# Kernel optimization log

Hardware: AMD Instinct MI355X
Metric: run time of the kernel (lower is better)

## Reference

```python
import jax, jax.numpy as jnp
import numpy as np

HIDDEN = 1024
D_FF = 2816
N_EXPERTS = 8
TOP_K = 2
TEMPERATURE = 1.0
LB_WEIGHT = 0.01


def setup_inputs() -> dict:
    key = jax.random.key(0)
    ks = jax.random.split(key, 5)
    scale_h = 1.0 / np.sqrt(HIDDEN)
    scale_f = 1.0 / np.sqrt(D_FF)
    x = jax.random.normal(ks[0], (2, 1024, HIDDEN), dtype=jnp.float32)
    gate_w = jax.random.normal(ks[1], (N_EXPERTS, HIDDEN), dtype=jnp.float32) * scale_h
    w1 = jax.random.normal(ks[2], (N_EXPERTS, HIDDEN, D_FF), dtype=jnp.float32) * scale_h  # gate proj
    w3 = jax.random.normal(ks[3], (N_EXPERTS, HIDDEN, D_FF), dtype=jnp.float32) * scale_h  # up proj
    w2 = jax.random.normal(ks[4], (N_EXPERTS, D_FF, HIDDEN), dtype=jnp.float32) * scale_f  # down proj
    return {"x": x, "gate_w": gate_w, "w1": w1, "w3": w3, "w2": w2}


def reference(x, gate_w, w1, w3, w2):
    B, S, H = x.shape
    xf = x.reshape(-1, H)                       # [T, H]
    T = xf.shape[0]

    # gating (eval mode: no routing noise)
    gate_logits = xf @ gate_w.T                 # [T, E]
    scaled = gate_logits / TEMPERATURE
    topk_vals, topk_idx = jax.lax.top_k(scaled, TOP_K)   # [T, K]
    topk_probs = jax.nn.softmax(topk_vals, axis=-1)      # [T, K]

    # dense combine weights: weight of expert e for token t (0 if not selected)
    onehot = jax.nn.one_hot(topk_idx, N_EXPERTS, dtype=xf.dtype)  # [T, K, E]
    comb = jnp.einsum("tke,tk->te", onehot, topk_probs)           # [T, E]

    # per-expert SwiGLU on all tokens, masked combine (math equals gather/scatter)
    h1 = jnp.einsum("th,ehf->etf", xf, w1)      # [E, T, F]
    h3 = jnp.einsum("th,ehf->etf", xf, w3)
    act = jax.nn.silu(h1) * h3                  # [E, T, F]
    y = jnp.einsum("etf,efh->eth", act, w2)     # [E, T, H]
    out = jnp.einsum("te,eth->th", comb, y)     # [T, H]

    # auxiliary load-balancing loss
    gate_probs = jax.nn.softmax(gate_logits, axis=-1)             # [T, E]
    expert_usage = onehot.sum(axis=(0, 1)) / (T * TOP_K + 1e-9)   # [E]
    gate_importance = gate_probs.mean(axis=0)                     # [E]
    aux = jnp.sum(expert_usage * gate_importance) * N_EXPERTS
    aux_loss = jnp.minimum(aux * LB_WEIGHT, 1.0)

    return out.reshape(B, S, H), aux_loss
```

## Files before the change

### kernel.cpp

```cpp
#include <hip/hip_runtime.h>
#include <hip/hip_bf16.h>
#include <math.h>


#define T_TOK 2048
#define HID   1024
#define DFF   2816
#define NE    8
#define ROWS  4096

typedef unsigned short u16;
typedef __attribute__((ext_vector_type(8))) short bf16x8;
typedef __attribute__((ext_vector_type(4))) float f32x4;

#define OFF_CNT    0
#define OFF_IMP    64
#define OFF_OFFS   128
#define OFF_TOPKI  256
#define OFF_TOPKP  (OFF_TOPKI + 16384)
#define OFF_BTOK   (OFF_TOPKP + 16384)
#define OFF_EPOS   (OFF_BTOK + 65536)
#define OFF_XB     (OFF_EPOS + 65536)
#define OFF_W1T    (OFF_XB + 4194304)
#define OFF_W3T    (OFF_W1T + 46137344)
#define OFF_W2T    (OFF_W3T + 46137344)
#define OFF_ACT    (OFF_W2T + 46137344)
#define WS_NEEDED  (OFF_ACT + 23068672)

__device__ __forceinline__ u16 f2bf(float f) {
    unsigned u = __float_as_uint(f);
    u = (u + 0x7fffu + ((u >> 16) & 1u)) >> 16;
    return (u16)u;
}

__device__ __forceinline__ void glds16(const void* g, void* l) {
    __builtin_amdgcn_global_load_lds(
        (const __attribute__((address_space(1))) unsigned int*)g,
        (__attribute__((address_space(3))) unsigned int*)l, 16, 0, 0);
}

__global__ void cvt_x_kernel(const float* __restrict__ x, u16* __restrict__ xb) {
    int i = blockIdx.x * 256 + threadIdx.x;
    float4 v = ((const float4*)x)[i];
    union { u16 s[4]; unsigned long long q; } o;
    o.s[0] = f2bf(v.x); o.s[1] = f2bf(v.y); o.s[2] = f2bf(v.z); o.s[3] = f2bf(v.w);
    ((unsigned long long*)xb)[i] = o.q;
}

__global__ void transpose_kernel(const float* __restrict__ in, u16* __restrict__ out,
                                 int K, int N) {
    __shared__ float tile[64][65];
    const float* ip = in + (size_t)blockIdx.z * K * N;
    u16* op = out + (size_t)blockIdx.z * K * N;
    int n0 = blockIdx.x * 64, k0 = blockIdx.y * 64;
    int tid = threadIdx.x;
#pragma unroll
    for (int p = 0; p < 4; ++p) {
        int row = p * 16 + (tid >> 4);
        int v = (tid & 15) * 4;
        float4 d = *(const float4*)(ip + (size_t)(k0 + row) * N + n0 + v);
        tile[row][v] = d.x; tile[row][v + 1] = d.y; tile[row][v + 2] = d.z; tile[row][v + 3] = d.w;
    }
    __syncthreads();
#pragma unroll
    for (int p = 0; p < 2; ++p) {
        int n = p * 32 + (tid >> 3);
        int g = (tid & 7) * 8;
        u16 o[8];
#pragma unroll
        for (int j = 0; j < 8; ++j) o[j] = f2bf(tile[g + j][n]);
        *(bf16x8*)(op + (size_t)(n0 + n) * K + k0 + g) = *(bf16x8*)o;
    }
}

__global__ void gating_kernel(const float* __restrict__ x, const float* __restrict__ gw,
                              int* __restrict__ topki, float* __restrict__ topkp,
                              float* __restrict__ imp) {
    __shared__ float s_imp[NE];
    int tid = threadIdx.x;
    if (tid < NE) s_imp[tid] = 0.f;
    __syncthreads();
    int lane = tid & 63;
    int t = blockIdx.x * 8 + (tid >> 6);
    float a[NE];
#pragma unroll
    for (int e = 0; e < NE; ++e) a[e] = 0.f;
#pragma unroll
    for (int c = 0; c < 16; ++c) {
        float xv = x[(size_t)t * HID + c * 64 + lane];
#pragma unroll
        for (int e = 0; e < NE; ++e) a[e] += xv * gw[e * HID + c * 64 + lane];
    }
#pragma unroll
    for (int e = 0; e < NE; ++e) {
#pragma unroll
        for (int off = 32; off > 0; off >>= 1) a[e] += __shfl_xor(a[e], off, 64);
    }
    if (lane == 0) {
        float v0 = -1e30f, v1 = -1e30f; int e0 = 0, e1 = 0;
#pragma unroll
        for (int e = 0; e < NE; ++e) {
            if (a[e] > v0) { v1 = v0; e1 = e0; v0 = a[e]; e0 = e; }
            else if (a[e] > v1) { v1 = a[e]; e1 = e; }
        }
        float p0 = 1.f / (1.f + expf(v1 - v0));
        topki[2 * t] = e0; topki[2 * t + 1] = e1;
        topkp[2 * t] = p0; topkp[2 * t + 1] = 1.f - p0;
        float s = 0.f, pe[NE];
#pragma unroll
        for (int e = 0; e < NE; ++e) { pe[e] = expf(a[e] - v0); s += pe[e]; }
        float inv = 1.f / s;
#pragma unroll
        for (int e = 0; e < NE; ++e) atomicAdd(&s_imp[e], pe[e] * inv);
    }
    __syncthreads();
    if (tid < NE) atomicAdd(&imp[tid], s_imp[tid]);
}

__global__ void compact_kernel(const int* __restrict__ topki,
                               int* __restrict__ cnt, int* __restrict__ btok,
                               int* __restrict__ epos) {
    int idx = blockIdx.x * 256 + threadIdx.x;
    int e = topki[idx];
    int pos = atomicAdd(&cnt[e], 1);
    btok[e * T_TOK + pos] = idx >> 1;
    epos[idx] = (e << 11) | pos;
}

__global__ void finalize_kernel(const int* __restrict__ cnt, const float* __restrict__ imp,
                                int* __restrict__ offs, float* __restrict__ aux_out) {
    if (threadIdx.x == 0) {
        int off = 0; float s = 0.f;
        for (int e = 0; e < NE; ++e) {
            offs[e] = off; off += cnt[e];
            s += ((float)cnt[e] / (4096.f + 1e-9f)) * (imp[e] / 2048.f);
        }
        aux_out[0] = fminf(s * 8.f * 0.01f, 1.f);
    }
}

__global__ __launch_bounds__(256, 2)
void gemm1_kernel(const u16* __restrict__ xb, const u16* __restrict__ w1t,
                  const u16* __restrict__ w3t, u16* __restrict__ act,
                  const int* __restrict__ btok, const int* __restrict__ cnt,
                  const int* __restrict__ offs) {
    int e = blockIdx.z;
    int n_e = cnt[e];
    int m0 = blockIdx.y * 128;
    if (m0 >= n_e) return;
    int nn0 = blockIdx.x * 128;
    int base = offs[e];

    __shared__ __align__(16) u16 As[128 * 32];
    __shared__ __align__(16) u16 B1s[128 * 32];
    __shared__ __align__(16) u16 B3s[128 * 32];

    int tid = threadIdx.x, lane = tid & 63, wv = tid >> 6;
    int wm = (wv >> 1) * 64, wn = (wv & 1) * 64;
    int l15 = lane & 15, quad = lane >> 4;

    int row0 = tid >> 2, row1 = 64 + row0;
    int q = (tid & 3) ^ ((tid >> 3) & 3);
    int sub = q * 8;
    int t0 = (m0 + row0 < n_e) ? btok[e * T_TOK + m0 + row0] : 0;
    int t1 = (m0 + row1 < n_e) ? btok[e * T_TOK + m0 + row1] : 0;
    const u16* ga0 = xb + (size_t)t0 * HID + sub;
    const u16* ga1 = xb + (size_t)t1 * HID + sub;
    const u16* g10 = w1t + ((size_t)e * DFF + nn0 + row0) * HID + sub;
    const u16* g11 = w1t + ((size_t)e * DFF + nn0 + row1) * HID + sub;
    const u16* g30 = w3t + ((size_t)e * DFF + nn0 + row0) * HID + sub;
    const u16* g31 = w3t + ((size_t)e * DFF + nn0 + row1) * HID + sub;
    u16* la0 = As  + (wv * 64) * 8;
    u16* la1 = As  + (256 + wv * 64) * 8;
    u16* l10 = B1s + (wv * 64) * 8;
    u16* l11 = B1s + (256 + wv * 64) * 8;
    u16* l30 = B3s + (wv * 64) * 8;
    u16* l31 = B3s + (256 + wv * 64) * 8;

    f32x4 acc1[4][4] = {}, acc3[4][4] = {};

    for (int k0 = 0; k0 < HID; k0 += 32) {
        glds16(ga0 + k0, la0); glds16(ga1 + k0, la1);
        glds16(g10 + k0, l10); glds16(g11 + k0, l11);
        glds16(g30 + k0, l30); glds16(g31 + k0, l31);
        __syncthreads();
        bf16x8 af[4];
#pragma unroll
        for (int i = 0; i < 4; ++i) {
            int R = wm + i * 16 + l15;
            af[i] = *(const bf16x8*)&As[R * 32 + (quad ^ ((R >> 1) & 3)) * 8];
        }
#pragma unroll
        for (int j = 0; j < 4; ++j) {
            int R = wn + j * 16 + l15;
            int so = R * 32 + (quad ^ ((R >> 1) & 3)) * 8;
            bf16x8 b1 = *(const bf16x8*)&B1s[so];
            bf16x8 b3 = *(const bf16x8*)&B3s[so];
#pragma unroll
            for (int i = 0; i < 4; ++i) {
                acc1[i][j] = __builtin_amdgcn_mfma_f32_16x16x32_bf16(af[i], b1, acc1[i][j], 0, 0, 0);
                acc3[i][j] = __builtin_amdgcn_mfma_f32_16x16x32_bf16(af[i], b3, acc3[i][j], 0, 0, 0);
            }
        }
        __syncthreads();
    }
#pragma unroll
    for (int i = 0; i < 4; ++i) {
#pragma unroll
        for (int r = 0; r < 4; ++r) {
            int m = m0 + wm + i * 16 + quad * 4 + r;
            if (m < n_e) {
#pragma unroll
                for (int j = 0; j < 4; ++j) {
                    float h1 = acc1[i][j][r], h3 = acc3[i][j][r];
                    float v = h1 / (1.f + expf(-h1)) * h3;
                    act[(size_t)(base + m) * DFF + nn0 + wn + j * 16 + l15] = f2bf(v);
                }
            }
        }
    }
}

__global__ __launch_bounds__(256, 4)
void gemm2_kernel(const u16* __restrict__ act, const u16* __restrict__ w2t,
                  float* __restrict__ ybuf, const int* __restrict__ cnt,
                  const int* __restrict__ offs) {
    int e = blockIdx.z;
    int n_e = cnt[e];
    int m0 = blockIdx.y * 64;
    if (m0 >= n_e) return;
    int nn0 = blockIdx.x * 128;
    int base = offs[e];

    __shared__ __align__(16) u16 As[64 * 32];
    __shared__ __align__(16) u16 Bs[128 * 32];

    int tid = threadIdx.x, lane = tid & 63, wv = tid >> 6;
    int wn = wv * 32;
    int l15 = lane & 15, quad = lane >> 4;

    int row0 = tid >> 2;
    int q = (tid & 3) ^ ((tid >> 3) & 3);
    int sub = q * 8;
    int ra = (m0 + row0 < n_e) ? (base + m0 + row0) : base;
    const u16* ga0 = act + (size_t)ra * DFF + sub;
    const u16* gb0 = w2t + ((size_t)e * HID + nn0 + row0) * DFF + sub;
    const u16* gb1 = w2t + ((size_t)e * HID + nn0 + 64 + row0) * DFF + sub;
    u16* la0 = As + (wv * 64) * 8;
    u16* lb0 = Bs + (wv * 64) * 8;
    u16* lb1 = Bs + (256 + wv * 64) * 8;

    f32x4 acc[4][2] = {};

    for (int k0 = 0; k0 < DFF; k0 += 32) {
        glds16(ga0 + k0, la0);
        glds16(gb0 + k0, lb0); glds16(gb1 + k0, lb1);
        __syncthreads();
        bf16x8 af[4];
#pragma unroll
        for (int i = 0; i < 4; ++i) {
            int R = i * 16 + l15;
            af[i] = *(const bf16x8*)&As[R * 32 + (quad ^ ((R >> 1) & 3)) * 8];
        }
#pragma unroll
        for (int j = 0; j < 2; ++j) {
            int R = wn + j * 16 + l15;
            bf16x8 bf = *(const bf16x8*)&Bs[R * 32 + (quad ^ ((R >> 1) & 3)) * 8];
#pragma unroll
            for (int i = 0; i < 4; ++i)
                acc[i][j] = __builtin_amdgcn_mfma_f32_16x16x32_bf16(af[i], bf, acc[i][j], 0, 0, 0);
        }
        __syncthreads();
    }
#pragma unroll
    for (int i = 0; i < 4; ++i) {
#pragma unroll
        for (int r = 0; r < 4; ++r) {
            int m = m0 + i * 16 + quad * 4 + r;
            if (m < n_e) {
#pragma unroll
                for (int j = 0; j < 2; ++j)
                    ybuf[(size_t)(base + m) * HID + nn0 + wn + j * 16 + l15] = acc[i][j][r];
            }
        }
    }
}

__global__ void combine_kernel(const float* __restrict__ ybuf, const int* __restrict__ epos,
                               const float* __restrict__ topkp, const int* __restrict__ offs,
                               float* __restrict__ out) {
    int t = blockIdx.x;
    int c = threadIdx.x * 4;
    int ep0 = epos[2 * t], ep1 = epos[2 * t + 1];
    int r0 = offs[ep0 >> 11] + (ep0 & 2047);
    int r1 = offs[ep1 >> 11] + (ep1 & 2047);
    float p0 = topkp[2 * t], p1 = topkp[2 * t + 1];
    float4 a = *(const float4*)&ybuf[(size_t)r0 * HID + c];
    float4 b = *(const float4*)&ybuf[(size_t)r1 * HID + c];
    float4 o;
    o.x = p0 * a.x + p1 * b.x; o.y = p0 * a.y + p1 * b.y;
    o.z = p0 * a.z + p1 * b.z; o.w = p0 * a.w + p1 * b.w;
    *(float4*)&out[(size_t)t * HID + c] = o;
}

extern "C" void kernel_launch(void* const* d_in, const int* in_sizes, int n_in,
                              void* d_out, int out_size, void* d_ws, size_t ws_size,
                              hipStream_t stream) {
    if (ws_size < (size_t)WS_NEEDED) return;

    const float* x  = (const float*)d_in[0];
    const float* gw = (const float*)d_in[1];
    const float* w1 = (const float*)d_in[2];
    const float* w3 = (const float*)d_in[3];
    const float* w2 = (const float*)d_in[4];
    float* out = (float*)d_out;

    char* ws = (char*)d_ws;
    int*   cnt   = (int*)(ws + OFF_CNT);
    float* imp   = (float*)(ws + OFF_IMP);
    int*   offs  = (int*)(ws + OFF_OFFS);
    int*   topki = (int*)(ws + OFF_TOPKI);
    float* topkp = (float*)(ws + OFF_TOPKP);
    int*   btok  = (int*)(ws + OFF_BTOK);
    int*   epos  = (int*)(ws + OFF_EPOS);
    u16*   xb    = (u16*)(ws + OFF_XB);
    u16*   w1t   = (u16*)(ws + OFF_W1T);
    u16*   w3t   = (u16*)(ws + OFF_W3T);
    u16*   w2t   = (u16*)(ws + OFF_W2T);
    u16*   actb  = (u16*)(ws + OFF_ACT);
    float* ybuf  = (float*)(ws + OFF_W1T);

    hipMemsetAsync(ws, 0, 256, stream);

    cvt_x_kernel<<<2048, 256, 0, stream>>>(x, xb);
    transpose_kernel<<<dim3(DFF / 64, HID / 64, NE), 256, 0, stream>>>(w1, w1t, HID, DFF);
    transpose_kernel<<<dim3(DFF / 64, HID / 64, NE), 256, 0, stream>>>(w3, w3t, HID, DFF);
    transpose_kernel<<<dim3(HID / 64, DFF / 64, NE), 256, 0, stream>>>(w2, w2t, DFF, HID);

    gating_kernel<<<T_TOK / 8, 512, 0, stream>>>(x, gw, topki, topkp, imp);
    compact_kernel<<<ROWS / 256, 256, 0, stream>>>(topki, cnt, btok, epos);
    finalize_kernel<<<1, 64, 0, stream>>>(cnt, imp, offs, out + (size_t)T_TOK * HID);

    gemm1_kernel<<<dim3(DFF / 128, T_TOK / 128, NE), 256, 0, stream>>>(
        xb, w1t, w3t, actb, btok, cnt, offs);
    gemm2_kernel<<<dim3(HID / 128, T_TOK / 64, NE), 256, 0, stream>>>(
        actb, w2t, ybuf, cnt, offs);
    combine_kernel<<<T_TOK, 256, 0, stream>>>(ybuf, epos, topkp, offs, out);
}
```

Measured before the change: 518.3 us.

## Double-buffer LDS tiles in both expert GEMMs to overlap loads with MFMA

Both grouped GEMM kernels now use ping-pong LDS buffers. The next K-slice is issued via global-to-LDS loads before computing on the current one, which removes one barrier per iteration. gemm2 also widens each stage to two 32-wide K slices (K step 64), which halves the barrier count. The cost is doubled or quadrupled LDS usage, so gemm2's launch bound occupancy drops from 4 to 3 blocks per CU, which could reduce latency hiding.

```diff
diff --git a/kernel.cpp b/kernel.cpp
--- a/kernel.cpp
+++ b/kernel.cpp
@@ -151,9 +151,9 @@
     int nn0 = blockIdx.x * 128;
     int base = offs[e];
 
-    __shared__ __align__(16) u16 As[128 * 32];
-    __shared__ __align__(16) u16 B1s[128 * 32];
-    __shared__ __align__(16) u16 B3s[128 * 32];
+    __shared__ __align__(16) u16 As[2 * 128 * 32];
+    __shared__ __align__(16) u16 B1s[2 * 128 * 32];
+    __shared__ __align__(16) u16 B3s[2 * 128 * 32];
 
     int tid = threadIdx.x, lane = tid & 63, wv = tid >> 6;
     int wm = (wv >> 1) * 64, wn = (wv & 1) * 64;
@@ -170,32 +170,39 @@
     const u16* g11 = w1t + ((size_t)e * DFF + nn0 + row1) * HID + sub;
     const u16* g30 = w3t + ((size_t)e * DFF + nn0 + row0) * HID + sub;
     const u16* g31 = w3t + ((size_t)e * DFF + nn0 + row1) * HID + sub;
-    u16* la0 = As  + (wv * 64) * 8;
-    u16* la1 = As  + (256 + wv * 64) * 8;
-    u16* l10 = B1s + (wv * 64) * 8;
-    u16* l11 = B1s + (256 + wv * 64) * 8;
-    u16* l30 = B3s + (wv * 64) * 8;
-    u16* l31 = B3s + (256 + wv * 64) * 8;
+    int wb0 = (wv * 64) * 8;
+    int wb1 = (256 + wv * 64) * 8;
 
     f32x4 acc1[4][4] = {}, acc3[4][4] = {};
 
+    glds16(ga0, As + wb0);  glds16(ga1, As + wb1);
+    glds16(g10, B1s + wb0); glds16(g11, B1s + wb1);
+    glds16(g30, B3s + wb0); glds16(g31, B3s + wb1);
+    __syncthreads();
+
+    int p = 0;
     for (int k0 = 0; k0 < HID; k0 += 32) {
-        glds16(ga0 + k0, la0); glds16(ga1 + k0, la1);
-        glds16(g10 + k0, l10); glds16(g11 + k0, l11);
-        glds16(g30 + k0, l30); glds16(g31 + k0, l31);
-        __syncthreads();
+        if (k0 + 32 < HID) {
+            int nb = (p ^ 1) * 128 * 32;
+            glds16(ga0 + k0 + 32, As + nb + wb0);  glds16(ga1 + k0 + 32, As + nb + wb1);
+            glds16(g10 + k0 + 32, B1s + nb + wb0); glds16(g11 + k0 + 32, B1s + nb + wb1);
+            glds16(g30 + k0 + 32, B3s + nb + wb0); glds16(g31 + k0 + 32, B3s + nb + wb1);
+        }
+        const u16* Ab  = As  + p * 128 * 32;
+        const u16* B1b = B1s + p * 128 * 32;
+        const u16* B3b = B3s + p * 128 * 32;
         bf16x8 af[4];
 #pragma unroll
         for (int i = 0; i < 4; ++i) {
             int R = wm + i * 16 + l15;
-            af[i] = *(const bf16x8*)&As[R * 32 + (quad ^ ((R >> 1) & 3)) * 8];
+            af[i] = *(const bf16x8*)&Ab[R * 32 + (quad ^ ((R >> 1) & 3)) * 8];
         }
 #pragma unroll
         for (int j = 0; j < 4; ++j) {
             int R = wn + j * 16 + l15;
             int so = R * 32 + (quad ^ ((R >> 1) & 3)) * 8;
-            bf16x8 b1 = *(const bf16x8*)&B1s[so];
-            bf16x8 b3 = *(const bf16x8*)&B3s[so];
+            bf16x8 b1 = *(const bf16x8*)&B1b[so];
+            bf16x8 b3 = *(const bf16x8*)&B3b[so];
 #pragma unroll
             for (int i = 0; i < 4; ++i) {
                 acc1[i][j] = __builtin_amdgcn_mfma_f32_16x16x32_bf16(af[i], b1, acc1[i][j], 0, 0, 0);
@@ -203,6 +210,7 @@
             }
         }
         __syncthreads();
+        p ^= 1;
     }
 #pragma unroll
     for (int i = 0; i < 4; ++i) {
@@ -221,7 +229,7 @@
     }
 }
 
-__global__ __launch_bounds__(256, 4)
+__global__ __launch_bounds__(256, 3)
 void gemm2_kernel(const u16* __restrict__ act, const u16* __restrict__ w2t,
                   float* __restrict__ ybuf, const int* __restrict__ cnt,
                   const int* __restrict__ offs) {
@@ -232,8 +240,8 @@
     int nn0 = blockIdx.x * 128;
     int base = offs[e];
 
-    __shared__ __align__(16) u16 As[64 * 32];
-    __shared__ __align__(16) u16 Bs[128 * 32];
+    __shared__ __align__(16) u16 As[2 * 2 * 64 * 32];
+    __shared__ __align__(16) u16 Bs[2 * 2 * 128 * 32];
 
     int tid = threadIdx.x, lane = tid & 63, wv = tid >> 6;
     int wn = wv * 32;
@@ -246,32 +254,51 @@
     const u16* ga0 = act + (size_t)ra * DFF + sub;
     const u16* gb0 = w2t + ((size_t)e * HID + nn0 + row0) * DFF + sub;
     const u16* gb1 = w2t + ((size_t)e * HID + nn0 + 64 + row0) * DFF + sub;
-    u16* la0 = As + (wv * 64) * 8;
-    u16* lb0 = Bs + (wv * 64) * 8;
-    u16* lb1 = Bs + (256 + wv * 64) * 8;
+    int wb = (wv * 64) * 8;
 
     f32x4 acc[4][2] = {};
 
-    for (int k0 = 0; k0 < DFF; k0 += 32) {
-        glds16(ga0 + k0, la0);
-        glds16(gb0 + k0, lb0); glds16(gb1 + k0, lb1);
+#define STAGE2(P, K0)                                                          \
+    do {                                                                       \
+        _Pragma("unroll")                                                      \
+        for (int h = 0; h < 2; ++h) {                                          \
+            int ab = (P) * 4096 + h * 2048;                                    \
+            int bb = (P) * 8192 + h * 4096;                                    \
+            glds16(ga0 + (K0) + h * 32, As + ab + wb);                         \
+            glds16(gb0 + (K0) + h * 32, Bs + bb + wb);                         \
+            glds16(gb1 + (K0) + h * 32, Bs + bb + 2048 + wb);                  \
+        }                                                                      \
+    } while (0)
+
+    STAGE2(0, 0);
+    __syncthreads();
+
+    int p = 0;
+    for (int k0 = 0; k0 < DFF; k0 += 64) {
+        if (k0 + 64 < DFF) STAGE2(p ^ 1, k0 + 64);
+#pragma unroll
+        for (int kk = 0; kk < 2; ++kk) {
+            const u16* Ab = As + p * 4096 + kk * 2048;
+            const u16* Bb = Bs + p * 8192 + kk * 4096;
+            bf16x8 af[4];
+#pragma unroll
+            for (int i = 0; i < 4; ++i) {
+                int R = i * 16 + l15;
+                af[i] = *(const bf16x8*)&Ab[R * 32 + (quad ^ ((R >> 1) & 3)) * 8];
+            }
+#pragma unroll
+            for (int j = 0; j < 2; ++j) {
+                int R = wn + j * 16 + l15;
+                bf16x8 bf = *(const bf16x8*)&Bb[R * 32 + (quad ^ ((R >> 1) & 3)) * 8];
+#pragma unroll
+                for (int i = 0; i < 4; ++i)
+                    acc[i][j] = __builtin_amdgcn_mfma_f32_16x16x32_bf16(af[i], bf, acc[i][j], 0, 0, 0);
+            }
+        }
         __syncthreads();
-        bf16x8 af[4];
-#pragma unroll
-        for (int i = 0; i < 4; ++i) {
-            int R = i * 16 + l15;
-            af[i] = *(const bf16x8*)&As[R * 32 + (quad ^ ((R >> 1) & 3)) * 8];
-        }
-#pragma unroll
-        for (int j = 0; j < 2; ++j) {
-            int R = wn + j * 16 + l15;
-            bf16x8 bf = *(const bf16x8*)&Bs[R * 32 + (quad ^ ((R >> 1) & 3)) * 8];
-#pragma unroll
-            for (int i = 0; i < 4; ++i)
-                acc[i][j] = __builtin_amdgcn_mfma_f32_16x16x32_bf16(af[i], bf, acc[i][j], 0, 0, 0);
-        }
-        __syncthreads();
-    }
+        p ^= 1;
+    }
+#undef STAGE2
 #pragma unroll
     for (int i = 0; i < 4; ++i) {
 #pragma unroll
```

Result: faster. 473.0 us (-8.8%).
